# Kernel tuning notes

Measured on AMD Instinct MI355X. Metric: run time of the kernel, lower is better.

## Reference

```python
import jax, jax.numpy as jnp
import numpy as np

# Config (matches init_kwargs)
IN_CH = 128
HID = 128
HEADS = 1
B, H, W = 8, 192, 192


def setup_inputs() -> dict:
    key = jax.random.key(0)
    ks = jax.random.split(key, 10)
    s = 0.05
    x = jax.random.normal(ks[0], (B, IN_CH, H, W), dtype=jnp.float32)
    # 1x1 conv weights stored as (out, in); bias (out,)
    Wq = jax.random.normal(ks[1], (HID, IN_CH), dtype=jnp.float32) * s
    bq = jax.random.normal(ks[2], (HID,), dtype=jnp.float32) * s
    Wk = jax.random.normal(ks[3], (HID, IN_CH), dtype=jnp.float32) * s
    bk = jax.random.normal(ks[4], (HID,), dtype=jnp.float32) * s
    Wv = jax.random.normal(ks[5], (HID, IN_CH), dtype=jnp.float32) * s
    bv = jax.random.normal(ks[6], (HID,), dtype=jnp.float32) * s
    Wo = jax.random.normal(ks[7], (IN_CH, HID), dtype=jnp.float32) * s
    bo = jax.random.normal(ks[8], (IN_CH,), dtype=jnp.float32) * s
    gamma = jax.random.normal(ks[9], (1,), dtype=jnp.float32) * 0.5
    return {"x": x, "Wq": Wq, "bq": bq, "Wk": Wk, "bk": bk,
            "Wv": Wv, "bv": bv, "Wo": Wo, "bo": bo, "gamma": gamma}


def _conv1x1(x, Wt, b):
    # x: (B, Cin, H, W); Wt: (Cout, Cin) -> (B, Cout, H, W)
    return jnp.einsum('oc,bchw->bohw', Wt, x) + b[None, :, None, None]


def reference(x, Wq, bq, Wk, bk, Wv, bv, Wo, bo, gamma):
    b, c, h, w = x.shape
    n = h * w
    d = HID // HEADS
    # q/k/v: (B, hidden, H, W) -> view(B, d, heads, N) -> (B*heads, d, N)
    def proj(Wt, bias):
        y = _conv1x1(x, Wt, bias).reshape(b, d, HEADS, n)
        return jnp.transpose(y, (0, 2, 1, 3)).reshape(b * HEADS, d, n)
    q = proj(Wq, bq)
    k = proj(Wk, bk)
    v = proj(Wv, bv)
    # NOTE: energy is d x d (channel attention), contracted over N. No scale.
    energy = jnp.einsum('bdn,ben->bde', q, k)        # (B*heads, d, d)
    attention = jax.nn.softmax(energy, axis=-1)
    attn_out = jnp.einsum('bde,ben->bdn', attention, v)  # (B*heads, d, N)
    attn_out = attn_out.reshape(b, HEADS, d, n)
    attn_out = jnp.transpose(attn_out, (0, 2, 1, 3)).reshape(b, HID, h, w)
    attn_out = _conv1x1(attn_out, Wo, bo)
    return gamma * attn_out + x
```

## Files before the change

### kernel.cpp

```cpp
#include <hip/hip_runtime.h>
#include <cstdint>
#include <cstddef>

#define NB  8
#define NC  128
#define NHW 36864

#define GOFF  0
#define SOFF  131072
#define TOFF  132096
#define ROFF  133120
#define CVOFF 264192
#define MBOFF 265216

typedef __attribute__((ext_vector_type(8))) short short8;
typedef __attribute__((ext_vector_type(4))) float f32x4;

static __device__ __forceinline__ f32x4 zero4(){ f32x4 v = {0.f,0.f,0.f,0.f}; return v; }

static __device__ __forceinline__ short bfbits(float f){
    union { __bf16 b; short s; } u; u.b = (__bf16)f; return u.s;
}
static __device__ __forceinline__ void cv2(float f, short& hb, short& lb){
    union { __bf16 b; short s; } u;
    u.b = (__bf16)f; hb = u.s;
    float hf = (float)u.b;
    u.b = (__bf16)(f - hf); lb = u.s;
}
static __device__ __forceinline__ float cv8(f32x4 v0, f32x4 v1, short8& h, short8& l){
    float ss = 0.f;
#pragma unroll
    for (int j=0;j<4;j++){
        short hb, lb;
        cv2(v0[j], hb, lb); h[j]   = hb; l[j]   = lb;
        cv2(v1[j], hb, lb); h[4+j] = hb; l[4+j] = lb;
        ss += v0[j] + v1[j];
    }
    return ss;
}

__global__ __launch_bounds__(256) void k_zero(float* __restrict__ p){
    const int i = (blockIdx.x*256 + threadIdx.x)*4;
    *(f32x4*)(p + i) = zero4();
}

#define GNT 36
#define GTS 4096

__global__ __launch_bounds__(512) void k_gram(const float* __restrict__ x,
                                              float* __restrict__ G,
                                              float* __restrict__ svec){
    __shared__ short Ls[3][2][GTS];
    const int b     = blockIdx.y;
    const int chunk = blockIdx.x;
    const int tid   = threadIdx.x;
    const int wid   = tid >> 6, lane = tid & 63;
    const int l16   = lane & 15, lgi = lane >> 4;
    const int sr    = tid >> 2;
    const int sc8   = (tid & 3) * 8;
    const int swzW  = ((sr >> 1) & 3) << 3;
    const int wIdx  = sr*32 + (sc8 ^ swzW);

    const int swzR  = ((l16 >> 1) & 3) << 3;
    const int cR    = (lgi*8) ^ swzR;
    const int raOff = (wid*16 + l16)*32 + cR;

    const float* xs = x + (size_t)b*NC*NHW + (size_t)sr*NHW + chunk*1152 + sc8;

    float srow = 0.f;
    f32x4 acc[8];
#pragma unroll
    for (int g=0;g<8;g++) acc[g] = zero4();

#define GR_STAGE(BUF, V0, V1)  { short8 h0,l0; srow += cv8(V0,V1,h0,l0); \
        *(short8*)&Ls[BUF][0][wIdx] = h0; *(short8*)&Ls[BUF][1][wIdx] = l0; }

#define GR_COMPUTE(BUF) { \
        const short* Lh = &Ls[BUF][0][0]; \
        const short* Ll = &Ls[BUF][1][0]; \
        short8 hA = *(const short8*)(Lh + raOff); \
        short8 lA = *(const short8*)(Ll + raOff); \
        _Pragma("unroll") \
        for (int g=0; g<8; g++){ \
            const int rb = (g*16 + l16)*32 + cR; \
            short8 hg  = *(const short8*)(Lh + rb); \
            short8 lg2 = *(const short8*)(Ll + rb); \
            acc[g] = __builtin_amdgcn_mfma_f32_16x16x32_bf16(hA, hg,  acc[g], 0,0,0); \
            acc[g] = __builtin_amdgcn_mfma_f32_16x16x32_bf16(hA, lg2, acc[g], 0,0,0); \
            acc[g] = __builtin_amdgcn_mfma_f32_16x16x32_bf16(lA, hg,  acc[g], 0,0,0); \
        } }

    {
        f32x4 v0 = *(const f32x4*)(xs);
        f32x4 v1 = *(const f32x4*)(xs+4);
        GR_STAGE(0, v0, v1);
        f32x4 u0 = *(const f32x4*)(xs+32);
        f32x4 u1 = *(const f32x4*)(xs+36);
        GR_STAGE(1, u0, u1);
    }
    f32x4 pA0 = *(const f32x4*)(xs + 64);
    f32x4 pA1 = *(const f32x4*)(xs + 68);
    f32x4 pB0, pB1;
    __syncthreads();

    int bm0 = 0, bm1 = 1, bm2 = 2;
    for (int tt = 0; tt < GNT-2; tt += 2){
        {
            const float* p = xs + (size_t)(tt+3)*32;
            pB0 = *(const f32x4*)(p);
            pB1 = *(const f32x4*)(p+4);
        }
        __builtin_amdgcn_sched_barrier(0);
        GR_COMPUTE(bm0);
        GR_STAGE(bm2, pA0, pA1);
        __syncthreads();
        if (tt+4 < GNT){
            const float* p = xs + (size_t)(tt+4)*32;
            pA0 = *(const f32x4*)(p);
            pA1 = *(const f32x4*)(p+4);
        }
        __builtin_amdgcn_sched_barrier(0);
        GR_COMPUTE(bm1);
        GR_STAGE(bm0, pB0, pB1);
        __syncthreads();
        const int tmp = bm2; bm2 = bm1; bm1 = bm0; bm0 = tmp;
    }
    GR_COMPUTE(bm0);
    GR_COMPUTE(bm1);

#undef GR_STAGE
#undef GR_COMPUTE

    float* Gb = G + (size_t)b*NC*NC;
#pragma unroll
    for (int g=0;g<8;g++){
#pragma unroll
        for (int r=0;r<4;r++){
            atomicAdd(&Gb[(size_t)(wid*16 + lgi*4 + r)*NC + g*16 + l16], acc[g][r]);
        }
    }
    srow += __shfl_xor(srow, 1);
    srow += __shfl_xor(srow, 2);
    if ((tid & 3) == 0) atomicAdd(&svec[b*NC + sr], srow);
}

__global__ __launch_bounds__(256) void k_energyav(const float* __restrict__ G,
        const float* __restrict__ svec,
        const float* __restrict__ Wq, const float* __restrict__ bq,
        const float* __restrict__ Wk, const float* __restrict__ bk,
        const float* __restrict__ bv, const float* __restrict__ Wv,
        float* __restrict__ R, float* __restrict__ tvec){
    const int b  = blockIdx.y;
    const int d0 = blockIdx.x * 16;
    const int tid = threadIdx.x;
    const int d  = tid & 15;
    const int ec = tid >> 4;

    __shared__ float Ps[16][128];
    __shared__ float Es[16][128];
    __shared__ float red[16][16];
    __shared__ float rowmax[16];
    __shared__ float rowsum[16];
    __shared__ float qs[16];

    const float* Wqrow = Wq + (size_t)(d0 + d)*NC;
    const float* sb = svec + b*NC;
#pragma unroll
    for (int i=0;i<8;i++){
        const int c = ec*8 + i;
        const float* Grow = G + ((size_t)b*NC + c)*NC;
        float a = 0.f;
        for (int c4=0;c4<32;c4++){
            f32x4 g4 = *(const f32x4*)(Grow + c4*4);
            f32x4 w4 = *(const f32x4*)(Wqrow + c4*4);
            a += g4[0]*w4[0] + g4[1]*w4[1] + g4[2]*w4[2] + g4[3]*w4[3];
        }
        Ps[d][c] = a;
    }
    if (ec == 0){
        float a = 0.f;
        for (int c4=0;c4<32;c4++){
            f32x4 w4 = *(const f32x4*)(Wqrow + c4*4);
            f32x4 s4 = *(const f32x4*)(sb + c4*4);
            a += w4[0]*s4[0] + w4[1]*s4[1] + w4[2]*s4[2] + w4[3]*s4[3];
        }
        qs[d] = a;
    }
    __syncthreads();
    const float bqd = bq[d0+d];
#pragma unroll
    for (int i=0;i<8;i++){
        const int e = ec*8 + i;
        const float* Wkrow = Wk + (size_t)e*NC;
        float ea = 0.f, ks = 0.f;
        for (int c4=0;c4<32;c4++){
            f32x4 w4 = *(const f32x4*)(Wkrow + c4*4);
            f32x4 p4 = *(const f32x4*)(&Ps[d][c4*4]);
            f32x4 s4 = *(const f32x4*)(sb + c4*4);
            ea += w4[0]*p4[0]+w4[1]*p4[1]+w4[2]*p4[2]+w4[3]*p4[3];
            ks += w4[0]*s4[0]+w4[1]*s4[1]+w4[2]*s4[2]+w4[3]*s4[3];
        }
        const float bke = bk[e];
        Es[d][e] = ea + bke*qs[d] + bqd*ks + (float)NHW*bqd*bke;
    }
    float m8 = -3.4e38f;
#pragma unroll
    for (int i=0;i<8;i++) m8 = fmaxf(m8, Es[d][ec*8+i]);
    red[d][ec] = m8;
    __syncthreads();
    if (tid < 16){
        float m = red[tid][0];
        for (int j=1;j<16;j++) m = fmaxf(m, red[tid][j]);
        rowmax[tid] = m;
    }
    __syncthreads();
    const float rm = rowmax[d];
    float s8 = 0.f;
#pragma unroll
    for (int i=0;i<8;i++){
        float ex = expf(Es[d][ec*8+i] - rm);
        Es[d][ec*8+i] = ex;
        s8 += ex;
    }
    red[d][ec] = s8;
    __syncthreads();
    if (tid < 16){
        float sm = 0.f;
        for (int j=0;j<16;j++) sm += red[tid][j];
        rowsum[tid] = sm;
    }
    __syncthreads();
    const float inv = 1.f / rowsum[d];
    float ta = 0.f;
#pragma unroll
    for (int i=0;i<8;i++){
        const int e = ec*8 + i;
        float av = Es[d][e] * inv;
        Es[d][e] = av;
        ta += av * bv[e];
    }
    red[d][ec] = ta;
    __syncthreads();
    if (tid < 16){
        float sm = 0.f;
        for (int j=0;j<16;j++) sm += red[tid][j];
        tvec[b*NC + d0 + tid] = sm;
    }
    const int c0 = ec*8;
    float racc[8];
#pragma unroll
    for (int i=0;i<8;i++) racc[i]=0.f;
    for (int e=0;e<NC;e++){
        const float av = Es[d][e];
        const float* wv = Wv + (size_t)e*NC + c0;
        f32x4 w0 = *(const f32x4*)wv;
        f32x4 w1 = *(const f32x4*)(wv+4);
        racc[0]+=av*w0[0]; racc[1]+=av*w0[1]; racc[2]+=av*w0[2]; racc[3]+=av*w0[3];
        racc[4]+=av*w1[0]; racc[5]+=av*w1[1]; racc[6]+=av*w1[2]; racc[7]+=av*w1[3];
    }
    float* Rrow = R + ((size_t)b*NC + d0 + d)*NC + c0;
#pragma unroll
    for (int i=0;i<8;i++) Rrow[i] = racc[i];
}

__global__ __launch_bounds__(256) void k_om(const float* __restrict__ R,
        const float* __restrict__ Wo, const float* __restrict__ bo,
        const float* __restrict__ tvec, const float* __restrict__ gamma,
        short* __restrict__ Mb_, float* __restrict__ cvg){
    const int b = blockIdx.y, o0 = blockIdx.x*16;
    const int tid = threadIdx.x, o = tid&15, cc = tid>>4;
    const int c0 = cc*8;
    const float* Worow = Wo + (size_t)(o0+o)*NC;
    const float* tb = tvec + b*NC;
    float a[8];
#pragma unroll
    for (int i=0;i<8;i++) a[i]=0.f;
    float cv = 0.f;
    for (int dd=0; dd<NC; dd++){
        const float wv = Worow[dd];
        const float* r = R + ((size_t)b*NC + dd)*NC + c0;
        f32x4 r0 = *(const f32x4*)r;
        f32x4 r1 = *(const f32x4*)(r+4);
        a[0]+=wv*r0[0]; a[1]+=wv*r0[1]; a[2]+=wv*r0[2]; a[3]+=wv*r0[3];
        a[4]+=wv*r1[0]; a[5]+=wv*r1[1]; a[6]+=wv*r1[2]; a[7]+=wv*r1[3];
        cv += wv*tb[dd];
    }
    const float gm = gamma[0];
    const int c   = o0 + o;
    const int cg  = c >> 4;
    const int kst = cc >> 2, lgv = cc & 3;
    const size_t idx = ((((size_t)b*8 + cg)*4 + kst)*64 + (lgv*16 + (c & 15)))*8;
    short8 hh;
#pragma unroll
    for (int i=0;i<8;i++){
        float val = gm*a[i] + ((c0 + i) == c ? 1.f : 0.f);
        hh[i] = bfbits(val);
    }
    *(short8*)(Mb_ + idx) = hh;
    if (cc == 0) cvg[b*NC + c] = gm*(cv + bo[c]);
}

__global__ __launch_bounds__(256, 4) void k_final(const float* __restrict__ x,
        const short* __restrict__ Mb_, const float* __restrict__ cvg,
        float* __restrict__ out){
    __shared__ short Xt[NC*128];
    const int b   = blockIdx.y;
    const int n0  = blockIdx.x * 128;
    const int tid = threadIdx.x;
    const int wid = tid >> 6, lane = tid & 63;
    const int l16 = lane & 15, lgi = lane >> 4;

    const int nr = tid & 31, mb8 = tid >> 5;
    const float* xs = x + (size_t)b*NC*NHW + n0 + nr*4;
#pragma unroll
    for (int rep=0; rep<2; rep++){
        const int m0 = rep*64 + mb8*8;
        const float* xm = xs + (size_t)m0*NHW;
        f32x4 v0 = *(const f32x4*)(xm);
        f32x4 v1 = *(const f32x4*)(xm + (size_t)1*NHW);
        f32x4 v2 = *(const f32x4*)(xm + (size_t)2*NHW);
        f32x4 v3 = *(const f32x4*)(xm + (size_t)3*NHW);
        f32x4 v4 = *(const f32x4*)(xm + (size_t)4*NHW);
        f32x4 v5 = *(const f32x4*)(xm + (size_t)5*NHW);
        f32x4 v6 = *(const f32x4*)(xm + (size_t)6*NHW);
        f32x4 v7 = *(const f32x4*)(xm + (size_t)7*NHW);
#pragma unroll
        for (int r=0;r<4;r++){
            short8 w;
            w[0]=bfbits(v0[r]); w[1]=bfbits(v1[r]); w[2]=bfbits(v2[r]); w[3]=bfbits(v3[r]);
            w[4]=bfbits(v4[r]); w[5]=bfbits(v5[r]); w[6]=bfbits(v6[r]); w[7]=bfbits(v7[r]);
            const int n = nr*4 + r;
            const int slot = (rep*8 + mb8) ^ ((n>>2)&15) ^ ((n&3)<<2);
            *(short8*)(&Xt[n*128 + slot*8]) = w;
        }
    }
    __syncthreads();

    f32x4 acc[2][8];
#pragma unroll
    for (int t=0;t<2;t++)
#pragma unroll
      for (int g=0;g<8;g++) acc[t][g]=zero4();

    const short* Mb = Mb_ + (size_t)b*16384;

#pragma unroll
    for (int ks=0; ks<4; ks++){
        const int nA0 = wid*32 + l16;
        const int nA1 = nA0 + 16;
        const int sl  = ks*4 + lgi;
        const int s0  = sl ^ ((nA0>>2)&15) ^ ((nA0&3)<<2);
        const int s1  = sl ^ ((nA1>>2)&15) ^ ((nA1&3)<<2);
        short8 a0 = *(const short8*)(&Xt[nA0*128 + s0*8]);
        short8 a1 = *(const short8*)(&Xt[nA1*128 + s1*8]);
#pragma unroll
        for (int cg=0; cg<8; cg++){
            short8 bh = *(const short8*)(Mb + (((size_t)cg*4 + ks)*64 + lane)*8);
            acc[0][cg] = __builtin_amdgcn_mfma_f32_16x16x32_bf16(a0, bh, acc[0][cg], 0,0,0);
            acc[1][cg] = __builtin_amdgcn_mfma_f32_16x16x32_bf16(a1, bh, acc[1][cg], 0,0,0);
        }
    }

    const float* cb = cvg + b*NC;
#pragma unroll
    for (int cg=0;cg<8;cg++){
        const int c = cg*16 + l16;
        const float ccv = cb[c];
        float* orow = &out[((size_t)b*NC + c)*NHW + n0 + wid*32 + lgi*4];
#pragma unroll
        for (int t=0;t<2;t++){
            f32x4 o = acc[t][cg];
            o[0]+=ccv; o[1]+=ccv; o[2]+=ccv; o[3]+=ccv;
            *(f32x4*)(orow + t*16) = o;
        }
    }
}

extern "C" void kernel_launch(void* const* d_in, const int* in_sizes, int n_in,
                              void* d_out, int out_size, void* d_ws, size_t ws_size,
                              hipStream_t stream){
    const float* x     = (const float*)d_in[0];
    const float* Wq    = (const float*)d_in[1];
    const float* bq    = (const float*)d_in[2];
    const float* Wk    = (const float*)d_in[3];
    const float* bk    = (const float*)d_in[4];
    const float* Wv    = (const float*)d_in[5];
    const float* bv    = (const float*)d_in[6];
    const float* Wo    = (const float*)d_in[7];
    const float* bo    = (const float*)d_in[8];
    const float* gamma = (const float*)d_in[9];
    float* out = (float*)d_out;

    float* w  = (float*)d_ws;
    float* G  = w + GOFF;
    float* S  = w + SOFF;
    float* T  = w + TOFF;
    float* R  = w + ROFF;
    float* CV = w + CVOFF;
    short* Mb = (short*)(w + MBOFF);

    k_zero    <<<dim3(129),     256, 0, stream>>>(G);

    k_gram    <<<dim3(32,  NB), 512, 0, stream>>>(x, G, S);
    k_energyav<<<dim3(8,   NB), 256, 0, stream>>>(G, S, Wq, bq, Wk, bk, bv, Wv, R, T);
    k_om      <<<dim3(8,   NB), 256, 0, stream>>>(R, Wo, bo, T, gamma, Mb, CV);
    k_final   <<<dim3(288, NB), 256, 0, stream>>>(x, Mb, CV, out);
}
```

Before: 173.0 us.

## Process two LDS tiles per barrier with a four-buffer pipeline in gram kernel

Restructures the k_gram main loop from a three-buffer, one-tile-per-barrier rotation to a fixed four-buffer scheme that computes two tiles between each __syncthreads and prefetches two tiles of x ahead into registers. This halves the number of block barriers and removes the rotating buffer indices, giving more MFMA work per synchronization. In exchange it raises LDS usage (from 48KB to 64KB per block) and register pressure from the extra prefetch registers, which may lower occupancy.

Measured after the change: 168.6 us. 2.6% less time.

```diff
diff --git a/kernel.cpp b/kernel.cpp
--- a/kernel.cpp
+++ b/kernel.cpp
@@ -50,7 +50,7 @@
 __global__ __launch_bounds__(512) void k_gram(const float* __restrict__ x,
                                               float* __restrict__ G,
                                               float* __restrict__ svec){
-    __shared__ short Ls[3][2][GTS];
+    __shared__ short Ls[4][2][GTS];
     const int b     = blockIdx.y;
     const int chunk = blockIdx.x;
     const int tid   = threadIdx.x;
@@ -98,35 +98,37 @@
         f32x4 u1 = *(const f32x4*)(xs+36);
         GR_STAGE(1, u0, u1);
     }
-    f32x4 pA0 = *(const f32x4*)(xs + 64);
-    f32x4 pA1 = *(const f32x4*)(xs + 68);
-    f32x4 pB0, pB1;
-    __syncthreads();
-
-    int bm0 = 0, bm1 = 1, bm2 = 2;
-    for (int tt = 0; tt < GNT-2; tt += 2){
+    f32x4 a0A = *(const f32x4*)(xs + 2*32);
+    f32x4 a0B = *(const f32x4*)(xs + 2*32 + 4);
+    f32x4 b0A = *(const f32x4*)(xs + 3*32);
+    f32x4 b0B = *(const f32x4*)(xs + 3*32 + 4);
+    f32x4 a1A, a1B, b1A, b1B;
+    __syncthreads();
+
+    for (int jp=0; jp<8; ++jp){
         {
-            const float* p = xs + (size_t)(tt+3)*32;
-            pB0 = *(const f32x4*)(p);
-            pB1 = *(const f32x4*)(p+4);
+            const float* p = xs + (size_t)(4*jp+4)*32;
+            a1A = *(const f32x4*)(p);       a1B = *(const f32x4*)(p+4);
+            b1A = *(const f32x4*)(p+32);    b1B = *(const f32x4*)(p+36);
         }
         __builtin_amdgcn_sched_barrier(0);
-        GR_COMPUTE(bm0);
-        GR_STAGE(bm2, pA0, pA1);
+        GR_COMPUTE(0); GR_COMPUTE(1);
+        GR_STAGE(2, a0A, a0B); GR_STAGE(3, b0A, b0B);
         __syncthreads();
-        if (tt+4 < GNT){
-            const float* p = xs + (size_t)(tt+4)*32;
-            pA0 = *(const f32x4*)(p);
-            pA1 = *(const f32x4*)(p+4);
+        {
+            const float* p = xs + (size_t)(4*jp+6)*32;
+            a0A = *(const f32x4*)(p);       a0B = *(const f32x4*)(p+4);
+            b0A = *(const f32x4*)(p+32);    b0B = *(const f32x4*)(p+36);
         }
         __builtin_amdgcn_sched_barrier(0);
-        GR_COMPUTE(bm1);
-        GR_STAGE(bm0, pB0, pB1);
+        GR_COMPUTE(2); GR_COMPUTE(3);
+        GR_STAGE(0, a1A, a1B); GR_STAGE(1, b1A, b1B);
         __syncthreads();
-        const int tmp = bm2; bm2 = bm1; bm1 = bm0; bm0 = tmp;
-    }
-    GR_COMPUTE(bm0);
-    GR_COMPUTE(bm1);
+    }
+    GR_COMPUTE(0); GR_COMPUTE(1);
+    GR_STAGE(2, a0A, a0B); GR_STAGE(3, b0A, b0B);
+    __syncthreads();
+    GR_COMPUTE(2); GR_COMPUTE(3);
 
 #undef GR_STAGE
 #undef GR_COMPUTE
```
